# Kernel optimization log

Measured on AMD Instinct MI355X. Metric: run time of the kernel, lower is better.

The kernel has to match this reference:

```python
import jax, jax.numpy as jnp
import numpy as np

D_MODEL = 768
N_HEADS = 12
D_HEAD = D_MODEL // N_HEADS


def setup_inputs() -> dict:
    key = jax.random.key(0)
    k1, k2, k3 = jax.random.split(key, 3)
    B, N = 32, 1024
    x = jax.random.normal(k1, (B, N, D_MODEL), dtype=jnp.float32)
    w_qkv = jax.random.normal(k2, (D_MODEL, 3 * D_MODEL), dtype=jnp.float32) * (D_MODEL ** -0.5)
    b_qkv = jnp.zeros((3 * D_MODEL,), dtype=jnp.float32)
    w_proj = jax.random.normal(k3, (D_MODEL, D_MODEL), dtype=jnp.float32) * (D_MODEL ** -0.5)
    b_proj = jnp.zeros((D_MODEL,), dtype=jnp.float32)
    return {"x": x, "w_qkv": w_qkv, "b_qkv": b_qkv, "w_proj": w_proj, "b_proj": b_proj}


def reference(x, w_qkv, b_qkv, w_proj, b_proj):
    B, N, C = x.shape
    H, Dh = N_HEADS, D_HEAD
    # qkv projection: (B,N,3C) -> (3,B,H,N,Dh)
    qkv = (x @ w_qkv + b_qkv).reshape(B, N, 3, H, Dh).transpose(2, 0, 3, 1, 4)
    q, k, v = qkv[0], qkv[1], qkv[2]
    scale = Dh ** -0.5
    attn = jnp.einsum('bhnd,bhmd->bhnm', q, k) * scale  # (B,H,N,N)
    attn = jax.nn.softmax(attn, axis=-1)
    out = jnp.einsum('bhnm,bhmd->bhnd', attn, v)  # (B,H,N,Dh)
    out = out.transpose(0, 2, 1, 3).reshape(B, N, C)
    return out @ w_proj + b_proj
```

## Files before the change

### kernel.cpp

```cpp
#include <hip/hip_runtime.h>
#include <hip/hip_bf16.h>
#include <math.h>

#define BQ   32
#define SEQ  1024
#define DM   768
#define NH   12
#define DH   64
#define CQKV 2304
#define MROWS (BQ * SEQ)

#define QSCALE 0.1803368801f

typedef __attribute__((ext_vector_type(8))) short  short8;
typedef __attribute__((ext_vector_type(4))) short  short4v;
typedef __attribute__((ext_vector_type(4))) float  floatx4;

using bf16 = __hip_bfloat16;

#define G2L(g, l) __builtin_amdgcn_global_load_lds(                              \
        (const __attribute__((address_space(1))) void*)(g),                      \
        (__attribute__((address_space(3))) void*)(l), 16, 0, 0)

#define WAVE_SYNC() __builtin_amdgcn_wave_barrier()
#define MFMA16(a, b, c) __builtin_amdgcn_mfma_f32_16x16x32_bf16((a), (b), (c), 0, 0, 0)

__global__ void cast_f32_bf16(const float* __restrict__ in, bf16* __restrict__ out,
                              int n4)
{
    int idx = blockIdx.x * blockDim.x + threadIdx.x;
    if (idx < n4) {
        float4 v = ((const float4*)in)[idx];
        bf16 o[4] = { __float2bfloat16(v.x), __float2bfloat16(v.y),
                      __float2bfloat16(v.z), __float2bfloat16(v.w) };
        ((ushort4*)out)[idx] = *(const ushort4*)o;
    }
}

__global__ void transpose_cast(const float* __restrict__ in, bf16* __restrict__ out,
                               int R, int C)
{
    int idx = blockIdx.x * blockDim.x + threadIdx.x;
    if (idx < R * C) {
        int r = idx / C, c = idx % C;
        out[(size_t)c * R + r] = __float2bfloat16(in[idx]);
    }
}

__device__ __forceinline__ void gemm_mainloop(
    const bf16* __restrict__ X, const bf16* __restrict__ WT,
    int m0, int n0, int t, int w, int lr, int lq,
    bf16* As, bf16* Bs, floatx4 acc[4][4])
{
    const int wm = (w >> 1) * 64, wn = (w & 1) * 64;
    const bf16* gA = X  + (size_t)(m0 + (t >> 2)) * DM + (t & 3) * 8;
    const bf16* gB = WT + (size_t)(n0 + (t >> 2)) * DM + (t & 3) * 8;
    bf16* lA = As + w * 512;
    bf16* lB = Bs + w * 512;

    for (int k0 = 0; k0 < DM; k0 += 32) {
        G2L(gA + k0,           lA);
        G2L(gA + 64 * DM + k0, lA + 2048);
        G2L(gB + k0,           lB);
        G2L(gB + 64 * DM + k0, lB + 2048);
        __syncthreads();
        short8 af[4], bfr[4];
        #pragma unroll
        for (int at = 0; at < 4; ++at)
            af[at] = *(const short8*)(As + (wm + at * 16 + lr) * 32 + lq * 8);
        #pragma unroll
        for (int bt = 0; bt < 4; ++bt)
            bfr[bt] = *(const short8*)(Bs + (wn + bt * 16 + lr) * 32 + lq * 8);
        #pragma unroll
        for (int at = 0; at < 4; ++at)
            #pragma unroll
            for (int bt = 0; bt < 4; ++bt)
                acc[at][bt] = MFMA16(af[at], bfr[bt], acc[at][bt]);
        __syncthreads();
    }
}

__global__ __launch_bounds__(256) void gemm_qkv(
    const bf16* __restrict__ X, const bf16* __restrict__ WT,
    const float* __restrict__ bias,
    bf16* __restrict__ Qo, bf16* __restrict__ Ko, bf16* __restrict__ Vt)
{
    __shared__ __align__(16) bf16 As[4096], Bs[4096];
    __shared__ __align__(16) bf16 Es[4][32][72];
    const int t = threadIdx.x, w = t >> 6, lane = t & 63;
    const int lr = lane & 15, lq = lane >> 4;
    const int id = blockIdx.x;
    const int xcd = id & 7, o = id >> 3;
    const int m0 = (xcd * 32 + o / 18) * 128;
    const int n0 = (o % 18) * 128;

    floatx4 acc[4][4] = {};
    gemm_mainloop(X, WT, m0, n0, t, w, lr, lq, As, Bs, acc);

    const int wm = (w >> 1) * 64, wn = (w & 1) * 64;
    const int cb = n0 + wn;
    const int which = cb / DM;
    const int hb    = (cb % DM) / DH;
    const int nbw   = m0 + wm;
    const int bb    = nbw >> 10, nloc = nbw & (SEQ - 1);
    const size_t head = (size_t)bb * NH + hb;
    const float qmul = (which == 0) ? QSCALE : 1.0f;

    if (which != 2) {
        bf16* Out = (which ? Ko : Qo) + (head * SEQ + nloc) * DH;
        #pragma unroll
        for (int c2 = 0; c2 < 2; ++c2) {
            #pragma unroll
            for (int ah = 0; ah < 2; ++ah) {
                const int at = c2 * 2 + ah;
                #pragma unroll
                for (int bt = 0; bt < 4; ++bt) {
                    const float bv = bias[cb + bt * 16 + lr];
                    #pragma unroll
                    for (int rr = 0; rr < 4; ++rr)
                        Es[w][ah * 16 + lq * 4 + rr][bt * 16 + lr] =
                            __float2bfloat16((acc[at][bt][rr] + bv) * qmul);
                }
            }
            WAVE_SYNC();
            #pragma unroll
            for (int i = 0; i < 4; ++i) {
                const int r = i * 8 + (lane >> 3), s = lane & 7;
                short8 vv = *(const short8*)(&Es[w][r][s * 8]);
                *(short8*)(Out + (size_t)(c2 * 32 + r) * DH + s * 8) = vv;
            }
            WAVE_SYNC();
        }
    } else {
        bf16* Out = Vt + head * DH * SEQ + nloc;
        #pragma unroll
        for (int c2 = 0; c2 < 2; ++c2) {
            #pragma unroll
            for (int bh = 0; bh < 2; ++bh) {
                const int bt = c2 * 2 + bh;
                const float bv = bias[cb + bt * 16 + lr];
                #pragma unroll
                for (int at = 0; at < 4; ++at)
                    #pragma unroll
                    for (int rr = 0; rr < 4; ++rr)
                        Es[w][bh * 16 + lr][at * 16 + lq * 4 + rr] =
                            __float2bfloat16(acc[at][bt][rr] + bv);
            }
            WAVE_SYNC();
            #pragma unroll
            for (int i = 0; i < 4; ++i) {
                const int r = i * 8 + (lane >> 3), s = lane & 7;
                short8 vv = *(const short8*)(&Es[w][r][s * 8]);
                *(short8*)(Out + (size_t)(c2 * 32 + r) * SEQ + s * 8) = vv;
            }
            WAVE_SYNC();
        }
    }
}

__global__ __launch_bounds__(256) void gemm_proj(
    const bf16* __restrict__ A, const bf16* __restrict__ WT,
    const float* __restrict__ bias, float* __restrict__ out)
{
    __shared__ __align__(16) bf16 As[4096], Bs[4096];
    const int t = threadIdx.x, w = t >> 6, lane = t & 63;
    const int lr = lane & 15, lq = lane >> 4;
    const int id = blockIdx.x;
    const int xcd = id & 7, o = id >> 3;
    const int m0 = (xcd * 32 + o / 6) * 128;
    const int n0 = (o % 6) * 128;

    floatx4 acc[4][4] = {};
    gemm_mainloop(A, WT, m0, n0, t, w, lr, lq, As, Bs, acc);

    const int wm = (w >> 1) * 64, wn = (w & 1) * 64;
    #pragma unroll
    for (int bt = 0; bt < 4; ++bt) {
        const float bv = bias[n0 + wn + bt * 16 + lr];
        #pragma unroll
        for (int at = 0; at < 4; ++at) {
            const int rg = m0 + wm + at * 16 + lq * 4;
            #pragma unroll
            for (int rr = 0; rr < 4; ++rr)
                out[(size_t)(rg + rr) * DM + n0 + wn + bt * 16 + lr] =
                    acc[at][bt][rr] + bv;
        }
    }
}

__global__ __launch_bounds__(256) void flash_attn(
    const bf16* __restrict__ Q, const bf16* __restrict__ K,
    const bf16* __restrict__ Vt, bf16* __restrict__ O)
{
    __shared__ __align__(16) bf16 Ks[2][2][64][32];
    __shared__ __align__(16) bf16 Vs[2][2][64][32];
    __shared__ __align__(16) bf16 Plds[4][32][72];
    const int w = threadIdx.x >> 6, lane = threadIdx.x & 63;
    const int lr = lane & 15, lq = lane >> 4;

    const int fid = blockIdx.x;
    const int g   = (fid & 7) + ((fid >> 6) << 3);
    const int x   = (fid >> 3) & 7;
    const int h   = g % NH, b = g / NH;
    const int qb  = x * 128 + w * 32;

    const bf16* Qh = Q  + (size_t)(b * NH + h) * SEQ * DH;
    const bf16* Kh = K  + (size_t)(b * NH + h) * SEQ * DH;
    const bf16* Vh = Vt + (size_t)(b * NH + h) * DH * SEQ;

    short8 bq[2][2];
    #pragma unroll
    for (int qs = 0; qs < 2; ++qs) {
        bq[qs][0] = *(const short8*)(Qh + (size_t)(qb + qs * 16 + lr) * DH + lq * 8);
        bq[qs][1] = *(const short8*)(Qh + (size_t)(qb + qs * 16 + lr) * DH + 32 + lq * 8);
    }

    floatx4 acc[2][4] = {};
    floatx4 lsum[2] = {};

    const int srow = lane >> 2;
    const int ssw  = ((lane & 3) ^ ((lane >> 3) & 3)) * 8;
    const int rsw  = (lr >> 1) & 3;

    const bf16* gsrc[4];
    bf16*       ldst[4];
    #pragma unroll
    for (int i = 0; i < 4; ++i) {
        const int idx = w * 4 + i;
        if (idx < 8) {
            const int hh = idx >> 2, gg = idx & 3;
            gsrc[i] = Kh + (size_t)(gg * 16 + srow) * DH + hh * 32 + ssw;
            ldst[i] = &Ks[0][hh][gg * 16][0];
        } else {
            const int vv = idx - 8, hh = vv >> 2, gg = vv & 3;
            gsrc[i] = Vh + (size_t)(gg * 16 + srow) * SEQ + hh * 32 + ssw;
            ldst[i] = &Vs[0][hh][gg * 16][0];
        }
    }
    const int gstep = (w < 2) ? 64 * DH : 64;

    auto stage = [&](int bi) {
        #pragma unroll
        for (int i = 0; i < 4; ++i) {
            G2L(gsrc[i], ldst[i] + bi * 4096);
            gsrc[i] += gstep;
        }
    };

    stage(0);
    __syncthreads();

    int cur = 0;
    for (int j0 = 0; j0 < SEQ; j0 += 64) {
        if (j0 + 64 < SEQ) stage(cur ^ 1);

        short8 ak[4][2];
        #pragma unroll
        for (int jt = 0; jt < 4; ++jt) {
            ak[jt][0] = *(const short8*)(&Ks[cur][0][jt * 16 + lr][(lq ^ rsw) * 8]);
            ak[jt][1] = *(const short8*)(&Ks[cur][1][jt * 16 + lr][(lq ^ rsw) * 8]);
        }
        #pragma unroll
        for (int qs = 0; qs < 2; ++qs) {
            #pragma unroll
            for (int jt = 0; jt < 4; ++jt) {
                floatx4 c = {};
                c = MFMA16(ak[jt][0], bq[qs][0], c);
                c = MFMA16(ak[jt][1], bq[qs][1], c);
                bf16 pk[4];
                #pragma unroll
                for (int r = 0; r < 4; ++r) {
                    float p = __builtin_amdgcn_exp2f(c[r]);
                    lsum[qs][r] += p;
                    pk[r] = __float2bfloat16(p);
                }
                *(short4v*)(&Plds[w][qs * 16 + lr][jt * 16 + lq * 4]) =
                    *(const short4v*)pk;
            }
        }
        WAVE_SYNC();

        short8 bv[4][2];
        #pragma unroll
        for (int dt = 0; dt < 4; ++dt) {
            bv[dt][0] = *(const short8*)(&Vs[cur][0][dt * 16 + lr][(lq ^ rsw) * 8]);
            bv[dt][1] = *(const short8*)(&Vs[cur][1][dt * 16 + lr][(lq ^ rsw) * 8]);
        }
        __builtin_amdgcn_s_setprio(1);
        #pragma unroll
        for (int qs = 0; qs < 2; ++qs) {
            short8 ap0 = *(const short8*)(&Plds[w][qs * 16 + lr][lq * 8]);
            short8 ap1 = *(const short8*)(&Plds[w][qs * 16 + lr][32 + lq * 8]);
            #pragma unroll
            for (int dt = 0; dt < 4; ++dt) {
                acc[qs][dt] = MFMA16(ap0, bv[dt][0], acc[qs][dt]);
                acc[qs][dt] = MFMA16(ap1, bv[dt][1], acc[qs][dt]);
            }
        }
        __builtin_amdgcn_s_setprio(0);

        __syncthreads();
        cur ^= 1;
    }

    float li[2];
    #pragma unroll
    for (int qs = 0; qs < 2; ++qs) {
        li[qs] = (lsum[qs][0] + lsum[qs][1]) + (lsum[qs][2] + lsum[qs][3]);
        li[qs] += __shfl_xor(li[qs], 16);
        li[qs] += __shfl_xor(li[qs], 32);
    }
    #pragma unroll
    for (int qs = 0; qs < 2; ++qs) {
        float inv[4];
        #pragma unroll
        for (int r = 0; r < 4; ++r)
            inv[r] = 1.f / __shfl(li[qs], lq * 4 + r);
        #pragma unroll
        for (int dt = 0; dt < 4; ++dt)
            #pragma unroll
            for (int r = 0; r < 4; ++r) {
                const int qi = qb + qs * 16 + lq * 4 + r;
                O[((size_t)b * SEQ + qi) * DM + h * DH + dt * 16 + lr] =
                    __float2bfloat16(acc[qs][dt][r] * inv[r]);
            }
    }
}

extern "C" void kernel_launch(void* const* d_in, const int* in_sizes, int n_in,
                              void* d_out, int out_size, void* d_ws, size_t ws_size,
                              hipStream_t stream)
{
    const float* x      = (const float*)d_in[0];
    const float* w_qkv  = (const float*)d_in[1];
    const float* b_qkv  = (const float*)d_in[2];
    const float* w_proj = (const float*)d_in[3];
    const float* b_proj = (const float*)d_in[4];
    float* out = (float*)d_out;

    bf16* ws = (bf16*)d_ws;
    size_t off = 0;
    bf16* wqkvT  = ws + off; off += (size_t)CQKV * DM;
    bf16* wprojT = ws + off; off += (size_t)DM * DM;
    bf16* Xb  = ws + off; off += (size_t)MROWS * DM;
    bf16* Qb  = ws + off; off += (size_t)BQ * NH * SEQ * DH;
    bf16* Kb  = ws + off; off += (size_t)BQ * NH * SEQ * DH;
    bf16* Vtb = ws + off; off += (size_t)BQ * NH * DH * SEQ;
    bf16* Ob  = ws + off; off += (size_t)MROWS * DM;

    cast_f32_bf16<<<(MROWS * DM / 4 + 255) / 256, 256, 0, stream>>>(x, Xb, MROWS * DM / 4);
    transpose_cast<<<(DM * CQKV + 255) / 256, 256, 0, stream>>>(w_qkv, wqkvT, DM, CQKV);
    transpose_cast<<<(DM * DM + 255) / 256, 256, 0, stream>>>(w_proj, wprojT, DM, DM);
    gemm_qkv<<<dim3(4608), 256, 0, stream>>>(Xb, wqkvT, b_qkv, Qb, Kb, Vtb);
    flash_attn<<<dim3(BQ * NH * (SEQ / 128)), 256, 0, stream>>>(Qb, Kb, Vtb, Ob);
    gemm_proj<<<dim3(1536), 256, 0, stream>>>(Ob, wprojT, b_proj, out);
}
```

Baseline: 523.5 us.

## Triple-buffer GEMM mainloop with 256x128 tiles, swizzled LDS and 8 waves

Replaces the single-buffered 128x128 GEMM mainloop, which issues loads and then synchronizes every 32-wide K step, with a 256x128 tile over 8 waves. The new loop uses 64-wide K stages, triple-buffered async global-to-LDS loads and explicit vmcnt waits, so memory latency overlaps with MFMA work. Both the global load addresses and the LDS reads are XOR-swizzled to avoid bank conflicts, and the MFMA section runs at raised wave priority. The cost is 144KB of dynamic LDS per block, which allows only one block per CU. It also fewer blocks in the grid and adds a one-time host-side attribute call.

New measurement: 505.6 us. -3.4%, faster.

```diff
diff --git a/kernel.cpp b/kernel.cpp
--- a/kernel.cpp
+++ b/kernel.cpp
@@ -9,6 +9,7 @@
 #define DH   64
 #define CQKV 2304
 #define MROWS (BQ * SEQ)
+#define NT   12
 
 #define QSCALE 0.1803368801f
 
@@ -47,55 +48,88 @@
     }
 }
 
-__device__ __forceinline__ void gemm_mainloop(
+__device__ __forceinline__ void mainloop256(
     const bf16* __restrict__ X, const bf16* __restrict__ WT,
-    int m0, int n0, int t, int w, int lr, int lq,
-    bf16* As, bf16* Bs, floatx4 acc[4][4])
+    int m0, int n0, int w, int lane, int lr, int lq,
+    bf16 (*Asm)[256][64], bf16 (*Bsm)[128][64], floatx4 acc[4][4])
 {
     const int wm = (w >> 1) * 64, wn = (w & 1) * 64;
-    const bf16* gA = X  + (size_t)(m0 + (t >> 2)) * DM + (t & 3) * 8;
-    const bf16* gB = WT + (size_t)(n0 + (t >> 2)) * DM + (t & 3) * 8;
-    bf16* lA = As + w * 512;
-    bf16* lB = Bs + w * 512;
-
-    for (int k0 = 0; k0 < DM; k0 += 32) {
-        G2L(gA + k0,           lA);
-        G2L(gA + 64 * DM + k0, lA + 2048);
-        G2L(gB + k0,           lB);
-        G2L(gB + 64 * DM + k0, lB + 2048);
-        __syncthreads();
-        short8 af[4], bfr[4];
-        #pragma unroll
-        for (int at = 0; at < 4; ++at)
-            af[at] = *(const short8*)(As + (wm + at * 16 + lr) * 32 + lq * 8);
-        #pragma unroll
-        for (int bt = 0; bt < 4; ++bt)
-            bfr[bt] = *(const short8*)(Bs + (wn + bt * 16 + lr) * 32 + lq * 8);
-        #pragma unroll
-        for (int at = 0; at < 4; ++at)
-            #pragma unroll
-            for (int bt = 0; bt < 4; ++bt)
-                acc[at][bt] = MFMA16(af[at], bfr[bt], acc[at][bt]);
-        __syncthreads();
-    }
-}
-
-__global__ __launch_bounds__(256) void gemm_qkv(
+    const int sr = lane >> 3;
+    const int ss = ((lane & 7) ^ sr) * 8;
+    const bf16* gA = X  + (size_t)(m0 + w * 8 + sr) * DM + ss;
+    const bf16* gB = WT + (size_t)(n0 + w * 8 + sr) * DM + ss;
+
+    auto stage = [&](int T) {
+        const int bI = T % 3;
+        #pragma unroll
+        for (int r = 0; r < 4; ++r)
+            G2L(gA + (size_t)(r * 64) * DM + T * 64, &Asm[bI][r * 64 + w * 8][0]);
+        #pragma unroll
+        for (int r = 0; r < 2; ++r)
+            G2L(gB + (size_t)(r * 64) * DM + T * 64, &Bsm[bI][r * 64 + w * 8][0]);
+    };
+
+    stage(0); stage(1);
+
+    #pragma unroll
+    for (int T = 0; T < NT; ++T) {
+        if (T + 2 < NT) stage(T + 2);
+        if      (T < NT - 2)  asm volatile("s_waitcnt vmcnt(12)" ::: "memory");
+        else if (T == NT - 2) asm volatile("s_waitcnt vmcnt(6)"  ::: "memory");
+        else                  asm volatile("s_waitcnt vmcnt(0)"  ::: "memory");
+        __builtin_amdgcn_s_barrier();
+        asm volatile("" ::: "memory");
+
+        const int bI = T % 3;
+        short8 af[4][2], bfr[4][2];
+        #pragma unroll
+        for (int m = 0; m < 4; ++m)
+            #pragma unroll
+            for (int ks = 0; ks < 2; ++ks)
+                af[m][ks] = *(const short8*)(
+                    &Asm[bI][wm + m * 16 + lr][((ks * 4 + lq) ^ (lr & 7)) * 8]);
+        #pragma unroll
+        for (int n = 0; n < 4; ++n)
+            #pragma unroll
+            for (int ks = 0; ks < 2; ++ks)
+                bfr[n][ks] = *(const short8*)(
+                    &Bsm[bI][wn + n * 16 + lr][((ks * 4 + lq) ^ (lr & 7)) * 8]);
+
+        __builtin_amdgcn_s_setprio(1);
+        #pragma unroll
+        for (int ks = 0; ks < 2; ++ks)
+            #pragma unroll
+            for (int m = 0; m < 4; ++m)
+                #pragma unroll
+                for (int n = 0; n < 4; ++n)
+                    acc[m][n] = MFMA16(af[m][ks], bfr[n][ks], acc[m][n]);
+        __builtin_amdgcn_s_setprio(0);
+
+        asm volatile("" ::: "memory");
+        __builtin_amdgcn_s_barrier();
+        asm volatile("" ::: "memory");
+    }
+}
+
+__global__ __launch_bounds__(512, 2) void gemm_qkv(
     const bf16* __restrict__ X, const bf16* __restrict__ WT,
     const float* __restrict__ bias,
     bf16* __restrict__ Qo, bf16* __restrict__ Ko, bf16* __restrict__ Vt)
 {
-    __shared__ __align__(16) bf16 As[4096], Bs[4096];
-    __shared__ __align__(16) bf16 Es[4][32][72];
+    extern __shared__ __align__(16) char smem[];
+    auto Asm = (bf16(*)[256][64])smem;
+    auto Bsm = (bf16(*)[128][64])(smem + 3 * 256 * 64 * 2);
+    auto Es  = (bf16(*)[32][72])smem;
+
     const int t = threadIdx.x, w = t >> 6, lane = t & 63;
     const int lr = lane & 15, lq = lane >> 4;
     const int id = blockIdx.x;
     const int xcd = id & 7, o = id >> 3;
-    const int m0 = (xcd * 32 + o / 18) * 128;
+    const int m0 = (xcd * 16 + o / 18) * 256;
     const int n0 = (o % 18) * 128;
 
     floatx4 acc[4][4] = {};
-    gemm_mainloop(X, WT, m0, n0, t, w, lr, lq, As, Bs, acc);
+    mainloop256(X, WT, m0, n0, w, lane, lr, lq, Asm, Bsm, acc);
 
     const int wm = (w >> 1) * 64, wn = (w & 1) * 64;
     const int cb = n0 + wn;
@@ -158,20 +192,23 @@
     }
 }
 
-__global__ __launch_bounds__(256) void gemm_proj(
+__global__ __launch_bounds__(512, 2) void gemm_proj(
     const bf16* __restrict__ A, const bf16* __restrict__ WT,
     const float* __restrict__ bias, float* __restrict__ out)
 {
-    __shared__ __align__(16) bf16 As[4096], Bs[4096];
+    extern __shared__ __align__(16) char smem[];
+    auto Asm = (bf16(*)[256][64])smem;
+    auto Bsm = (bf16(*)[128][64])(smem + 3 * 256 * 64 * 2);
+
     const int t = threadIdx.x, w = t >> 6, lane = t & 63;
     const int lr = lane & 15, lq = lane >> 4;
     const int id = blockIdx.x;
     const int xcd = id & 7, o = id >> 3;
-    const int m0 = (xcd * 32 + o / 6) * 128;
+    const int m0 = (xcd * 16 + o / 6) * 256;
     const int n0 = (o % 6) * 128;
 
     floatx4 acc[4][4] = {};
-    gemm_mainloop(A, WT, m0, n0, t, w, lr, lq, As, Bs, acc);
+    mainloop256(A, WT, m0, n0, w, lane, lr, lq, Asm, Bsm, acc);
 
     const int wm = (w >> 1) * 64, wn = (w & 1) * 64;
     #pragma unroll
@@ -348,10 +385,19 @@
     bf16* Vtb = ws + off; off += (size_t)BQ * NH * DH * SEQ;
     bf16* Ob  = ws + off; off += (size_t)MROWS * DM;
 
+    static bool attr_done = false;
+    if (!attr_done) {
+        (void)hipFuncSetAttribute((const void*)gemm_qkv,
+                hipFuncAttributeMaxDynamicSharedMemorySize, 147456);
+        (void)hipFuncSetAttribute((const void*)gemm_proj,
+                hipFuncAttributeMaxDynamicSharedMemorySize, 147456);
+        attr_done = true;
+    }
+
     cast_f32_bf16<<<(MROWS * DM / 4 + 255) / 256, 256, 0, stream>>>(x, Xb, MROWS * DM / 4);
     transpose_cast<<<(DM * CQKV + 255) / 256, 256, 0, stream>>>(w_qkv, wqkvT, DM, CQKV);
     transpose_cast<<<(DM * DM + 255) / 256, 256, 0, stream>>>(w_proj, wprojT, DM, DM);
-    gemm_qkv<<<dim3(4608), 256, 0, stream>>>(Xb, wqkvT, b_qkv, Qb, Kb, Vtb);
+    gemm_qkv<<<dim3(2304), 512, 147456, stream>>>(Xb, wqkvT, b_qkv, Qb, Kb, Vtb);
     flash_attn<<<dim3(BQ * NH * (SEQ / 128)), 256, 0, stream>>>(Qb, Kb, Vtb, Ob);
-    gemm_proj<<<dim3(1536), 256, 0, stream>>>(Ob, wprojT, b_proj, out);
-}
+    gemm_proj<<<dim3(768), 512, 147456, stream>>>(Ob, wprojT, b_proj, out);
+}
```
